# Performance work log

Hardware: AMD Instinct MI355X
Metric: run time of the kernel (lower is better)

## Reference

```python
import jax, jax.numpy as jnp
import numpy as np

DIM = 768
NUM_HEADS = 12
SCALE = 1.0 / (DIM ** 0.5)  # NOTE: source scales by 1/sqrt(dim), not 1/sqrt(head_dim)


def setup_inputs() -> dict:
    key = jax.random.key(0)
    k_x, k_qkv, k_ow, k_ob = jax.random.split(key, 4)
    b, n = 8, 1024
    x = jax.random.normal(k_x, (b, n, DIM), dtype=jnp.float32)
    # torch Linear weight is [out, in]; we store jax-style [in, out]
    w_qkv = jax.random.normal(k_qkv, (DIM, 3 * DIM), dtype=jnp.float32) * (DIM ** -0.5)
    w_out = jax.random.normal(k_ow, (DIM, DIM), dtype=jnp.float32) * (DIM ** -0.5)
    b_out = jax.random.normal(k_ob, (DIM,), dtype=jnp.float32) * 0.01
    return {"x": x, "w_qkv": w_qkv, "w_out": w_out, "b_out": b_out}


def reference(x, w_qkv, w_out, b_out):
    b, n, c = x.shape
    h = NUM_HEADS
    hd = c // h
    qkv = (x @ w_qkv).reshape(b, n, 3, h, hd)
    q, k, v = jnp.moveaxis(qkv, 2, 0)          # each [b, n, h, hd]
    q = jnp.swapaxes(q, 1, 2)                  # [b, h, n, hd]
    k = jnp.swapaxes(k, 1, 2)
    v = jnp.swapaxes(v, 1, 2)
    dot = jnp.einsum('bhqd,bhkd->bhqk', q, k) * SCALE
    attn = jax.nn.softmax(dot, axis=-1)        # attn_dropout p=0 -> identity
    out = jnp.einsum('bhqk,bhkd->bhqd', attn, v)
    out = jnp.swapaxes(out, 1, 2).reshape(b, n, c)
    return out @ w_out + b_out                 # proj_dropout p=0 -> identity
```

## Files before the change

### kernel.cpp

```cpp
#include <hip/hip_runtime.h>

#define DEV __device__ __forceinline__

typedef __bf16 bf16x8 __attribute__((ext_vector_type(8)));
typedef float  f32x4  __attribute__((ext_vector_type(4)));

static constexpr float SCALE = 0.036084391824351615f;
static constexpr float L2E   = 1.4426950408889634f;

DEV unsigned short f2bf(float f) {
  return __builtin_bit_cast(unsigned short, (__bf16)f);
}
DEV unsigned int pack2(float a, float b) {
  return (unsigned int)f2bf(a) | ((unsigned int)f2bf(b) << 16);
}

#define GLDS16(gp, lp) \
  __builtin_amdgcn_global_load_lds((__attribute__((address_space(1))) void*)(gp), \
                                   (__attribute__((address_space(3))) void*)(lp), 16, 0, 0)


__global__ __launch_bounds__(256) void k_cvt_bf16(const float* __restrict__ in,
                                                  unsigned short* __restrict__ out,
                                                  int n8) {
  int i = blockIdx.x * 256 + threadIdx.x;
  if (i >= n8) return;
  const float4* p = (const float4*)in + (size_t)i * 2;
  float4 a = p[0], b = p[1];
  uint4 r;
  r.x = pack2(a.x, a.y); r.y = pack2(a.z, a.w);
  r.z = pack2(b.x, b.y); r.w = pack2(b.z, b.w);
  ((uint4*)out)[i] = r;
}

__global__ __launch_bounds__(256) void k_transpose_w(const float* __restrict__ in,
                                                     unsigned short* __restrict__ out,
                                                     int R, int C) {
  __shared__ float tile[64][65];
  int c0 = blockIdx.x * 64, r0 = blockIdx.y * 64;
  int t = threadIdx.x, tr = t >> 6, tc = t & 63;
#pragma unroll
  for (int i = 0; i < 64; i += 4)
    tile[i + tr][tc] = in[(size_t)(r0 + i + tr) * C + c0 + tc];
  __syncthreads();
#pragma unroll
  for (int i = 0; i < 64; i += 4)
    out[(size_t)(c0 + i + tr) * R + r0 + tc] = f2bf(tile[tc][i + tr]);
}

template <int MODE>
__global__ __launch_bounds__(256) void k_gemm(const unsigned short* __restrict__ A,
                                              const unsigned short* __restrict__ BT,
                                              void* __restrict__ out0,
                                              unsigned short* __restrict__ Kb,
                                              unsigned short* __restrict__ VTb,
                                              const float* __restrict__ bias) {
  __shared__ __align__(16) char smem[32768];
  char* As = smem;
  char* Bs = smem + 16384;
  const int tid = threadIdx.x;
  const int wave = tid >> 6, lane = tid & 63;
  const int g = lane >> 4, l15 = lane & 15;
  const int wrow = wave >> 1, wcol = wave & 1;

  int id = blockIdx.y * gridDim.x + blockIdx.x;
  int per_xcd = (gridDim.x * gridDim.y) >> 3;
  int id2 = (id & 7) * per_xcd + (id >> 3);
  const int bm = id2 / gridDim.x, bn = id2 % gridDim.x;

  f32x4 acc[4][4] = {};
  const unsigned short* Abase = A + (size_t)bm * 128 * 768;
  const unsigned short* Bbase = BT + (size_t)bn * 128 * 768;

  for (int kt = 0; kt < 12; ++kt) {
    const int k0 = kt * 64;
#pragma unroll
    for (int i = 0; i < 4; ++i) {
      int q = i * 256 + tid;
      int row = q >> 3, c = q & 7;
      int cs = c ^ (row & 7);
      GLDS16(Abase + (size_t)row * 768 + k0 + cs * 8, As + (i * 256 + wave * 64) * 16);
      GLDS16(Bbase + (size_t)row * 768 + k0 + cs * 8, Bs + (i * 256 + wave * 64) * 16);
    }
    __syncthreads();
    __builtin_amdgcn_s_setprio(1);
#pragma unroll
    for (int kk = 0; kk < 2; ++kk) {
      bf16x8 af[4], bfr[4];
#pragma unroll
      for (int mi = 0; mi < 4; ++mi) {
        int r = wrow * 64 + mi * 16 + l15;
        af[mi] = *(const bf16x8*)(As + r * 128 + (((kk * 4 + g) ^ (r & 7)) * 16));
      }
#pragma unroll
      for (int ni = 0; ni < 4; ++ni) {
        int r = wcol * 64 + ni * 16 + l15;
        bfr[ni] = *(const bf16x8*)(Bs + r * 128 + (((kk * 4 + g) ^ (r & 7)) * 16));
      }
#pragma unroll
      for (int mi = 0; mi < 4; ++mi)
#pragma unroll
        for (int ni = 0; ni < 4; ++ni)
          acc[mi][ni] = __builtin_amdgcn_mfma_f32_16x16x32_bf16(af[mi], bfr[ni], acc[mi][ni], 0, 0, 0);
    }
    __builtin_amdgcn_s_setprio(0);
    __syncthreads();
  }

  const int row0 = bm * 128 + wrow * 64;
  const int col0 = bn * 128 + wcol * 64;
#pragma unroll
  for (int mi = 0; mi < 4; ++mi) {
#pragma unroll
    for (int ni = 0; ni < 4; ++ni) {
      int col = col0 + ni * 16 + l15;
      if (MODE == 0) {
        int which = col / 768;
        int hd = col - which * 768;
        int head = hd >> 6, d = hd & 63;
        int rowm0 = row0 + mi * 16 + g * 4;
        int bi = rowm0 >> 10, np = rowm0 & 1023;
        if (which == 0) {
#pragma unroll
          for (int j = 0; j < 4; ++j)
            ((unsigned short*)out0)[((size_t)(bi * 12 + head) * 1024 + np + j) * 64 + d] =
                f2bf(acc[mi][ni][j] * (SCALE * L2E));
        } else if (which == 1) {
#pragma unroll
          for (int j = 0; j < 4; ++j)
            Kb[((size_t)(bi * 12 + head) * 1024 + np + j) * 64 + d] = f2bf(acc[mi][ni][j]);
        } else {
          ushort4 w;
          w.x = f2bf(acc[mi][ni][0]); w.y = f2bf(acc[mi][ni][1]);
          w.z = f2bf(acc[mi][ni][2]); w.w = f2bf(acc[mi][ni][3]);
          *(ushort4*)(VTb + ((size_t)(bi * 12 + head) * 64 + d) * 1024 + np) = w;
        }
      } else {
        float bz = bias[col];
#pragma unroll
        for (int j = 0; j < 4; ++j) {
          int rowm = row0 + mi * 16 + g * 4 + j;
          ((float*)out0)[(size_t)rowm * 768 + col] = acc[mi][ni][j] + bz;
        }
      }
    }
  }
}

__global__ __launch_bounds__(256) void k_attn(const unsigned short* __restrict__ Qb,
                                              const unsigned short* __restrict__ Kb,
                                              const unsigned short* __restrict__ VTb,
                                              unsigned short* __restrict__ Ao) {
  __shared__ __align__(16) char smem[49152];
  char* Ps = smem + 32768;
  const int tid = threadIdx.x, wave = tid >> 6, lane = tid & 63;
  const int g = lane >> 4, l15 = lane & 15;
  const int bh = blockIdx.x % 96, qt = blockIdx.x / 96;
  const int qbase = qt * 128 + wave * 32;
  const unsigned short* Kp = Kb + (size_t)bh * 65536;
  const unsigned short* Vp = VTb + (size_t)bh * 65536;

  auto STAGE = [&](int buf, int kt) {
#pragma unroll
    for (int i = 0; i < 2; ++i) {
      int q = i * 256 + tid;
      int row = q >> 3, c = q & 7;
      int cs = c ^ (row & 7);
      GLDS16(Kp + (size_t)(kt * 64 + row) * 64 + cs * 8,
             smem + buf * 8192 + (i * 256 + wave * 64) * 16);
      GLDS16(Vp + (size_t)row * 1024 + kt * 64 + cs * 8,
             smem + 16384 + buf * 8192 + (i * 256 + wave * 64) * 16);
    }
  };

  bf16x8 aq[2][2];
#pragma unroll
  for (int mi = 0; mi < 2; ++mi)
#pragma unroll
    for (int kk = 0; kk < 2; ++kk)
      aq[mi][kk] = *(const bf16x8*)(Qb + (size_t)bh * 65536 +
                                    (size_t)(qbase + mi * 16 + l15) * 64 + kk * 32 + g * 8);

  f32x4 o[2][4] = {};
  float lrow[2] = {0.f, 0.f};
  char* Pw = Ps + wave * 4096;

  STAGE(0, 0);
  __syncthreads();
  int cur = 0;

  for (int kt = 0; kt < 16; ++kt) {
    if (kt < 15) STAGE(cur ^ 1, kt + 1);
    char* Ks = smem + cur * 8192;
    char* Vs = smem + 16384 + cur * 8192;

    f32x4 st[2][4] = {};
    __builtin_amdgcn_s_setprio(1);
#pragma unroll
    for (int dk = 0; dk < 2; ++dk) {
      bf16x8 ka[4];
#pragma unroll
      for (int kf = 0; kf < 4; ++kf) {
        int r = kf * 16 + l15;
        ka[kf] = *(const bf16x8*)(Ks + r * 128 + (((dk * 4 + g) ^ (r & 7)) * 16));
      }
#pragma unroll
      for (int qf = 0; qf < 2; ++qf)
#pragma unroll
        for (int kf = 0; kf < 4; ++kf)
          st[qf][kf] = __builtin_amdgcn_mfma_f32_16x16x32_bf16(ka[kf], aq[qf][dk], st[qf][kf], 0, 0, 0);
    }
    __builtin_amdgcn_s_setprio(0);

#pragma unroll
    for (int qf = 0; qf < 2; ++qf) {
      float sum = 0.f;
#pragma unroll
      for (int kf = 0; kf < 4; ++kf)
#pragma unroll
        for (int j = 0; j < 4; ++j) {
          float e = __builtin_amdgcn_exp2f(st[qf][kf][j]);
          st[qf][kf][j] = e;
          sum += e;
        }
      lrow[qf] += sum;

      int qrow = qf * 16 + l15;
      char* prow = Pw + qrow * 128;
#pragma unroll
      for (int kf = 0; kf < 4; ++kf) {
        unsigned off = kf * 32 + g * 8;
        off = (off & 15u) | ((((off >> 4) ^ (unsigned)qrow) & 7u) << 4);
        uint2 w;
        w.x = pack2(st[qf][kf][0], st[qf][kf][1]);
        w.y = pack2(st[qf][kf][2], st[qf][kf][3]);
        *(uint2*)(prow + off) = w;
      }
    }

    __builtin_amdgcn_s_setprio(1);
#pragma unroll
    for (int kk = 0; kk < 2; ++kk) {
      bf16x8 vb[4];
#pragma unroll
      for (int df = 0; df < 4; ++df) {
        int r = df * 16 + l15;
        vb[df] = *(const bf16x8*)(Vs + r * 128 + (((kk * 4 + g) ^ (r & 7)) * 16));
      }
#pragma unroll
      for (int qf = 0; qf < 2; ++qf) {
        int qrow = qf * 16 + l15;
        bf16x8 pa = *(const bf16x8*)(Pw + qrow * 128 + ((((kk * 4 + g) ^ qrow) & 7) << 4));
#pragma unroll
        for (int df = 0; df < 4; ++df)
          o[qf][df] = __builtin_amdgcn_mfma_f32_16x16x32_bf16(pa, vb[df], o[qf][df], 0, 0, 0);
      }
    }
    __builtin_amdgcn_s_setprio(0);

    __syncthreads();
    cur ^= 1;
  }

  const int b_idx = bh / 12, h = bh - b_idx * 12;
#pragma unroll
  for (int qf = 0; qf < 2; ++qf) {
    lrow[qf] += __shfl_xor(lrow[qf], 16);
    lrow[qf] += __shfl_xor(lrow[qf], 32);
    float linv = 1.0f / lrow[qf];
#pragma unroll
    for (int j = 0; j < 4; ++j) {
      float lj = __shfl(linv, g * 4 + j);
      int qrow = qbase + qf * 16 + g * 4 + j;
#pragma unroll
      for (int df = 0; df < 4; ++df) {
        int col = h * 64 + df * 16 + l15;
        Ao[(size_t)(b_idx * 1024 + qrow) * 768 + col] = f2bf(o[qf][df][j] * lj);
      }
    }
  }
}


extern "C" void kernel_launch(void* const* d_in, const int* in_sizes, int n_in,
                              void* d_out, int out_size, void* d_ws, size_t ws_size,
                              hipStream_t stream) {
  const float* x     = (const float*)d_in[0];
  const float* w_qkv = (const float*)d_in[1];
  const float* w_out = (const float*)d_in[2];
  const float* b_out = (const float*)d_in[3];

  char* ws = (char*)d_ws;
  size_t off = 0;
  auto alloc = [&](size_t bytes) {
    void* p = ws + off;
    off += (bytes + 255) & ~(size_t)255;
    return p;
  };
  unsigned short* xb    = (unsigned short*)alloc(8192ull * 768 * 2);
  unsigned short* wqkvT = (unsigned short*)alloc(2304ull * 768 * 2);
  unsigned short* woutT = (unsigned short*)alloc(768ull * 768 * 2);
  unsigned short* Qb    = (unsigned short*)alloc(96ull * 1024 * 64 * 2);
  unsigned short* Kbf   = (unsigned short*)alloc(96ull * 1024 * 64 * 2);
  unsigned short* VTb   = (unsigned short*)alloc(96ull * 1024 * 64 * 2);
  unsigned short* Aob   = (unsigned short*)alloc(96ull * 1024 * 64 * 2);

  k_cvt_bf16<<<3072, 256, 0, stream>>>(x, xb, 786432);
  k_transpose_w<<<dim3(36, 12), 256, 0, stream>>>(w_qkv, wqkvT, 768, 2304);
  k_transpose_w<<<dim3(12, 12), 256, 0, stream>>>(w_out, woutT, 768, 768);
  k_gemm<0><<<dim3(18, 64), 256, 0, stream>>>(xb, wqkvT, Qb, Kbf, VTb, nullptr);
  k_attn<<<768, 256, 0, stream>>>(Qb, Kbf, VTb, Aob);
  k_gemm<1><<<dim3(6, 64), 256, 0, stream>>>(Aob, woutT, d_out, nullptr, nullptr, b_out);
}
```

Baseline: 112.4 us.

## Switch attention to 32x32x16 MFMA and pass P through registers instead of LDS

The attention kernel now uses 32x32x16 bf16 MFMAs. Computing S^T with K as the A operand leaves each lane holding one query's scores as an accumulator, so after exp2 and bf16 packing the P tile is rebuilt into the A-operand layout with cross-half lane shuffles. This removes the per-wave LDS round trip for P and drops shared memory from 48KB to 32KB. The cost is extra shuffle and select instructions and a different register footprint. Correctness depends on the lane permutation matching the 32x32 MFMA operand layout.

```diff
diff --git a/kernel.cpp b/kernel.cpp
--- a/kernel.cpp
+++ b/kernel.cpp
@@ -4,6 +4,8 @@
 
 typedef __bf16 bf16x8 __attribute__((ext_vector_type(8)));
 typedef float  f32x4  __attribute__((ext_vector_type(4)));
+typedef float  f32x16 __attribute__((ext_vector_type(16)));
+typedef unsigned int u32x4 __attribute__((ext_vector_type(4)));
 
 static constexpr float SCALE = 0.036084391824351615f;
 static constexpr float L2E   = 1.4426950408889634f;
@@ -151,10 +153,9 @@
                                               const unsigned short* __restrict__ Kb,
                                               const unsigned short* __restrict__ VTb,
                                               unsigned short* __restrict__ Ao) {
-  __shared__ __align__(16) char smem[49152];
-  char* Ps = smem + 32768;
+  __shared__ __align__(16) char smem[32768];
   const int tid = threadIdx.x, wave = tid >> 6, lane = tid & 63;
-  const int g = lane >> 4, l15 = lane & 15;
+  const int hi = lane >> 5, q31 = lane & 31;
   const int bh = blockIdx.x % 96, qt = blockIdx.x / 96;
   const int qbase = qt * 128 + wave * 32;
   const unsigned short* Kp = Kb + (size_t)bh * 65536;
@@ -173,17 +174,14 @@
     }
   };
 
-  bf16x8 aq[2][2];
-#pragma unroll
-  for (int mi = 0; mi < 2; ++mi)
-#pragma unroll
-    for (int kk = 0; kk < 2; ++kk)
-      aq[mi][kk] = *(const bf16x8*)(Qb + (size_t)bh * 65536 +
-                                    (size_t)(qbase + mi * 16 + l15) * 64 + kk * 32 + g * 8);
-
-  f32x4 o[2][4] = {};
-  float lrow[2] = {0.f, 0.f};
-  char* Pw = Ps + wave * 4096;
+  bf16x8 aq[4];
+#pragma unroll
+  for (int dk = 0; dk < 4; ++dk)
+    aq[dk] = *(const bf16x8*)(Qb + (size_t)bh * 65536 +
+                              (size_t)(qbase + q31) * 64 + dk * 16 + hi * 8);
+
+  f32x16 o0 = {}, o1 = {};
+  float lsum = 0.f;
 
   STAGE(0, 0);
   __syncthreads();
@@ -194,89 +192,75 @@
     char* Ks = smem + cur * 8192;
     char* Vs = smem + 16384 + cur * 8192;
 
-    f32x4 st[2][4] = {};
-    __builtin_amdgcn_s_setprio(1);
-#pragma unroll
-    for (int dk = 0; dk < 2; ++dk) {
-      bf16x8 ka[4];
-#pragma unroll
-      for (int kf = 0; kf < 4; ++kf) {
-        int r = kf * 16 + l15;
-        ka[kf] = *(const bf16x8*)(Ks + r * 128 + (((dk * 4 + g) ^ (r & 7)) * 16));
-      }
-#pragma unroll
-      for (int qf = 0; qf < 2; ++qf)
-#pragma unroll
-        for (int kf = 0; kf < 4; ++kf)
-          st[qf][kf] = __builtin_amdgcn_mfma_f32_16x16x32_bf16(ka[kf], aq[qf][dk], st[qf][kf], 0, 0, 0);
-    }
-    __builtin_amdgcn_s_setprio(0);
-
-#pragma unroll
-    for (int qf = 0; qf < 2; ++qf) {
-      float sum = 0.f;
-#pragma unroll
-      for (int kf = 0; kf < 4; ++kf)
-#pragma unroll
-        for (int j = 0; j < 4; ++j) {
-          float e = __builtin_amdgcn_exp2f(st[qf][kf][j]);
-          st[qf][kf][j] = e;
-          sum += e;
+#pragma unroll
+    for (int sub = 0; sub < 2; ++sub) {
+      f32x16 st = {};
+      __builtin_amdgcn_s_setprio(1);
+#pragma unroll
+      for (int dk = 0; dk < 4; ++dk) {
+        int r = sub * 32 + q31;
+        bf16x8 ka = *(const bf16x8*)(Ks + r * 128 + (((dk * 2 + hi) ^ (r & 7)) * 16));
+        st = __builtin_amdgcn_mfma_f32_32x32x16_bf16(ka, aq[dk], st, 0, 0, 0);
+      }
+      __builtin_amdgcn_s_setprio(0);
+
+      float ex[16];
+#pragma unroll
+      for (int r2 = 0; r2 < 16; ++r2) ex[r2] = __builtin_amdgcn_exp2f(st[r2]);
+      float s0 = (ex[0] + ex[1]) + (ex[2] + ex[3]);
+      float s1 = (ex[4] + ex[5]) + (ex[6] + ex[7]);
+      float s2 = (ex[8] + ex[9]) + (ex[10] + ex[11]);
+      float s3 = (ex[12] + ex[13]) + (ex[14] + ex[15]);
+      lsum += (s0 + s1) + (s2 + s3);
+
+      unsigned w00 = pack2(ex[0], ex[1]),   w01 = pack2(ex[2], ex[3]);
+      unsigned w10 = pack2(ex[4], ex[5]),   w11 = pack2(ex[6], ex[7]);
+      unsigned w20 = pack2(ex[8], ex[9]),   w21 = pack2(ex[10], ex[11]);
+      unsigned w30 = pack2(ex[12], ex[13]), w31 = pack2(ex[14], ex[15]);
+      unsigned r00 = __shfl_xor((int)w00, 32), r01 = __shfl_xor((int)w01, 32);
+      unsigned r10 = __shfl_xor((int)w10, 32), r11 = __shfl_xor((int)w11, 32);
+      unsigned r20 = __shfl_xor((int)w20, 32), r21 = __shfl_xor((int)w21, 32);
+      unsigned r30 = __shfl_xor((int)w30, 32), r31 = __shfl_xor((int)w31, 32);
+
+      __builtin_amdgcn_s_setprio(1);
+#pragma unroll
+      for (int s = 0; s < 2; ++s) {
+        u32x4 au;
+        if (s == 0) {
+          au[0] = hi ? r10 : w00; au[1] = hi ? r11 : w01;
+          au[2] = hi ? w10 : r00; au[3] = hi ? w11 : r01;
+        } else {
+          au[0] = hi ? r30 : w20; au[1] = hi ? r31 : w21;
+          au[2] = hi ? w30 : r20; au[3] = hi ? w31 : r21;
         }
-      lrow[qf] += sum;
-
-      int qrow = qf * 16 + l15;
-      char* prow = Pw + qrow * 128;
-#pragma unroll
-      for (int kf = 0; kf < 4; ++kf) {
-        unsigned off = kf * 32 + g * 8;
-        off = (off & 15u) | ((((off >> 4) ^ (unsigned)qrow) & 7u) << 4);
-        uint2 w;
-        w.x = pack2(st[qf][kf][0], st[qf][kf][1]);
-        w.y = pack2(st[qf][kf][2], st[qf][kf][3]);
-        *(uint2*)(prow + off) = w;
-      }
-    }
-
-    __builtin_amdgcn_s_setprio(1);
-#pragma unroll
-    for (int kk = 0; kk < 2; ++kk) {
-      bf16x8 vb[4];
-#pragma unroll
-      for (int df = 0; df < 4; ++df) {
-        int r = df * 16 + l15;
-        vb[df] = *(const bf16x8*)(Vs + r * 128 + (((kk * 4 + g) ^ (r & 7)) * 16));
-      }
-#pragma unroll
-      for (int qf = 0; qf < 2; ++qf) {
-        int qrow = qf * 16 + l15;
-        bf16x8 pa = *(const bf16x8*)(Pw + qrow * 128 + ((((kk * 4 + g) ^ qrow) & 7) << 4));
-#pragma unroll
-        for (int df = 0; df < 4; ++df)
-          o[qf][df] = __builtin_amdgcn_mfma_f32_16x16x32_bf16(pa, vb[df], o[qf][df], 0, 0, 0);
-      }
-    }
-    __builtin_amdgcn_s_setprio(0);
+        bf16x8 pa = __builtin_bit_cast(bf16x8, au);
+        int ch = sub * 4 + s * 2 + hi;
+        int vr0 = q31, vr1 = 32 + q31;
+        bf16x8 vb0 = *(const bf16x8*)(Vs + vr0 * 128 + ((ch ^ (vr0 & 7)) * 16));
+        bf16x8 vb1 = *(const bf16x8*)(Vs + vr1 * 128 + ((ch ^ (vr1 & 7)) * 16));
+        o0 = __builtin_amdgcn_mfma_f32_32x32x16_bf16(pa, vb0, o0, 0, 0, 0);
+        o1 = __builtin_amdgcn_mfma_f32_32x32x16_bf16(pa, vb1, o1, 0, 0, 0);
+      }
+      __builtin_amdgcn_s_setprio(0);
+    }
 
     __syncthreads();
     cur ^= 1;
   }
 
+  lsum += __shfl_xor(lsum, 32);
+  float linv = 1.0f / lsum;
   const int b_idx = bh / 12, h = bh - b_idx * 12;
 #pragma unroll
-  for (int qf = 0; qf < 2; ++qf) {
-    lrow[qf] += __shfl_xor(lrow[qf], 16);
-    lrow[qf] += __shfl_xor(lrow[qf], 32);
-    float linv = 1.0f / lrow[qf];
+  for (int m = 0; m < 4; ++m) {
 #pragma unroll
     for (int j = 0; j < 4; ++j) {
-      float lj = __shfl(linv, g * 4 + j);
-      int qrow = qbase + qf * 16 + g * 4 + j;
-#pragma unroll
-      for (int df = 0; df < 4; ++df) {
-        int col = h * 64 + df * 16 + l15;
-        Ao[(size_t)(b_idx * 1024 + qrow) * 768 + col] = f2bf(o[qf][df][j] * lj);
-      }
+      int qr = j + 8 * m + 4 * hi;
+      float lj = __shfl(linv, qr);
+      int reg = m * 4 + j;
+      size_t base = (size_t)(b_idx * 1024 + qbase + qr) * 768 + h * 64 + q31;
+      Ao[base]      = f2bf(o0[reg] * lj);
+      Ao[base + 32] = f2bf(o1[reg] * lj);
     }
   }
 }
```

Result: no change. 112.5 us (+0.1%).
